# Kernel tuning notes

Measured on AMD Instinct MI355X. Metric: run time of the kernel, lower is better.

## Reference

```python
import jax, jax.numpy as jnp
import numpy as np

B, S, W = 32, 128, 20
WV, CV = 50000, 128
WD, CE = 300, 50
KS = (2, 3, 4, 5)
NF = 64
TOTF = NF * len(KS)
CF = 300
H = 512
L = 9
LP = L + 2
START, END = L, L + 1
NEG = -10000.0


def setup_inputs():
    key = jax.random.key(0)
    ks = jax.random.split(key, 40)
    def nrm(i, shape, scale=0.1):
        return jax.random.normal(ks[i], shape, dtype=jnp.float32) * scale
    inp = {}
    inp['token_ids'] = jax.random.randint(ks[0], (B, S), 0, WV)
    inp['char_ids'] = jax.random.randint(ks[1], (B, S, W), 0, CV)
    lens = jnp.sort(jax.random.randint(ks[2], (B,), S // 2, S + 1))[::-1]
    inp['lens'] = lens.astype(jnp.int32)
    inp['labels'] = jax.random.randint(ks[3], (B, S), 0, L)
    inp['word_embed'] = nrm(4, (WV, WD))
    inp['char_embed'] = nrm(5, (CV, CE))
    for j, k in enumerate(KS):
        inp['conv_w%d' % k] = nrm(6 + j, (k, CE, NF))
        inp['conv_b%d' % k] = nrm(10 + j, (NF,))
    inp['ff_w'] = nrm(14, (CF, TOTF))
    inp['ff_b'] = nrm(15, (CF,))
    inp['wgate_w'] = nrm(16, (WD, WD))
    inp['cgate_w'] = nrm(17, (CF, CF))
    inp['gate_w'] = nrm(18, (WD, WD))
    inp['wih_f'] = nrm(19, (4 * H, WD))
    inp['whh_f'] = nrm(20, (4 * H, H))
    inp['b_f'] = nrm(21, (4 * H,))
    inp['wih_b'] = nrm(22, (4 * H, WD))
    inp['whh_b'] = nrm(23, (4 * H, H))
    inp['b_b'] = nrm(24, (4 * H,))
    inp['out_w'] = nrm(25, (L, 2 * H))
    inp['out_b'] = nrm(26, (L,))
    inp['trn'] = nrm(27, (LP, LP))
    return inp


def _char_cnn(char_ids, char_embed, convs):
    x = char_embed[char_ids.reshape(-1, W)]  # [B*S, W, CE]
    feats = []
    for w, b in convs:
        y = jax.lax.conv_general_dilated(x, w, (1,), 'VALID',
                                         dimension_numbers=('NWC', 'WIO', 'NWC')) + b
        feats.append(jnp.max(jax.nn.relu(y), axis=1))  # max over time -> [B*S, NF]
    return jnp.concatenate(feats, axis=1)  # [B*S, TOTF]


def _run_lstm(x, mask, wih, whh, b, reverse):
    # x [B,S,D], mask bool [B,S]; padded steps freeze state and emit zeros (packed-seq semantics)
    xg = jnp.einsum('bsd,gd->bsg', x, wih) + b  # [B,S,4H]
    xg_t = jnp.swapaxes(xg, 0, 1)               # [S,B,4H]
    m_t = jnp.swapaxes(mask, 0, 1)[..., None]   # [S,B,1]
    h0 = jnp.zeros((x.shape[0], H), x.dtype)
    def step(carry, inp):
        h, c = carry
        g_t, m = inp
        g = g_t + h @ whh.T
        i, f, gg, o = jnp.split(g, 4, axis=-1)  # torch gate order i,f,g,o
        cn = jax.nn.sigmoid(f) * c + jax.nn.sigmoid(i) * jnp.tanh(gg)
        hn = jax.nn.sigmoid(o) * jnp.tanh(cn)
        h = jnp.where(m, hn, h)
        c = jnp.where(m, cn, c)
        return (h, c), jnp.where(m, hn, 0.0)
    _, out = jax.lax.scan(step, (h0, h0), (xg_t, m_t), reverse=reverse)
    return jnp.swapaxes(out, 0, 1)  # [B,S,H]


def _crf_norm(logits, mask, trn):
    # logits [B,S,LP]; trn[i,j] = score(prev=j -> next=i)
    alpha = logits[:, 0] + trn[:, START][None, :]
    lt = jnp.swapaxes(logits, 0, 1)[1:]                 # [S-1,B,LP]
    mt = jnp.swapaxes(mask, 0, 1)[1:][..., None]        # [S-1,B,1]
    def step(alpha, inp):
        lg, m = inp
        new = jax.scipy.special.logsumexp(alpha[:, None, :] + trn[None], axis=2) + lg
        return jnp.where(m, new, alpha), None
    alpha, _ = jax.lax.scan(step, alpha, (lt, mt))
    return jax.scipy.special.logsumexp(alpha + trn[END][None, :], axis=1)


def _crf_gold(logits, labels, lens, mask, trn):
    fm = mask.astype(logits.dtype)
    emit = jnp.take_along_axis(logits, labels[..., None], axis=2)[..., 0]
    emit = jnp.sum(emit * fm, axis=1)
    trans = trn[labels[:, 1:], labels[:, :-1]] * fm[:, 1:]
    first = trn[labels[:, 0], START]
    last_lab = jnp.take_along_axis(labels, (lens - 1)[:, None], axis=1)[:, 0]
    return emit + jnp.sum(trans, axis=1) + first + trn[END, last_lab]


def reference(token_ids, char_ids, lens, labels, word_embed, char_embed,
              conv_w2, conv_b2, conv_w3, conv_b3, conv_w4, conv_b4, conv_w5, conv_b5,
              ff_w, ff_b, wgate_w, cgate_w, gate_w,
              wih_f, whh_f, b_f, wih_b, whh_b, b_b, out_w, out_b, trn):
    word_in = word_embed[token_ids]                               # [B,S,WD]
    convs = [(conv_w2, conv_b2), (conv_w3, conv_b3), (conv_w4, conv_b4), (conv_w5, conv_b5)]
    ch = _char_cnn(char_ids, char_embed, convs)                   # [B*S,TOTF]
    char_in = (ch @ ff_w.T + ff_b).reshape(B, S, CF)              # CharCNNFF output
    g = jax.nn.sigmoid(jnp.tanh(word_in @ wgate_w.T + char_in @ cgate_w.T) @ gate_w.T)
    feats = g * word_in + (1.0 - g) * char_in                     # gated fusion (dropout = eval identity)
    mask = jnp.arange(S)[None, :] < lens[:, None]                 # [B,S] bool
    hf = _run_lstm(feats, mask, wih_f, whh_f, b_f, False)
    hb = _run_lstm(feats, mask, wih_b, whh_b, b_b, True)
    lstm_out = jnp.concatenate([hf, hb], axis=-1)                 # [B,S,2H]
    logits = lstm_out @ out_w.T + out_b                           # [B,S,L]
    pads = jnp.full((B, S, 2), NEG, logits.dtype)
    logits = jnp.concatenate([logits, pads], axis=2)              # pad_logits -> [B,S,LP]
    norm = _crf_norm(logits, mask, trn)
    gold = _crf_gold(logits, labels, lens, mask, trn)
    loglik = gold - norm
    return (loglik, logits)
```

## Files before the change

### kernel.cpp

```cpp
#include <hip/hip_runtime.h>

#define NB    32
#define SEQ   128
#define WCH   20
#define CED   50
#define NFLT  64
#define WDIM  300
#define HD    512
#define NWORD 4096
#define LPAD  11
#define NEGV  -10000.0f
#define LSTM_BLOCKS 16

typedef float f32x4 __attribute__((ext_vector_type(4)));
typedef __bf16 bf16x8 __attribute__((ext_vector_type(8)));
typedef unsigned short u16x8 __attribute__((ext_vector_type(8)));

static __device__ __forceinline__ unsigned short f2bf(float f) {
  unsigned u = __builtin_bit_cast(unsigned, f);
  u += 0x7fffu + ((u >> 16) & 1u);
  return (unsigned short)(u >> 16);
}
static __device__ __forceinline__ float bf2f(unsigned short s) {
  unsigned u = ((unsigned)s) << 16;
  return __builtin_bit_cast(float, u);
}
static __device__ __forceinline__ float sigf(float x) { return 1.0f / (1.0f + expf(-x)); }
static __device__ __forceinline__ void unpk(unsigned u, float& a, float& b) {
  a = bf2f((unsigned short)(u & 0xffffu));
  b = bf2f((unsigned short)(u >> 16));
}

__global__ __launch_bounds__(256) void conv_kernel(
    const int* __restrict__ char_ids, const float* __restrict__ char_embed,
    const float* __restrict__ w2, const float* __restrict__ b2,
    const float* __restrict__ w3, const float* __restrict__ b3,
    const float* __restrict__ w4, const float* __restrict__ b4,
    const float* __restrict__ w5, const float* __restrict__ b5,
    float* __restrict__ ch)
{
  __shared__ __align__(16) float xT[CED][WCH];
  int wi = blockIdx.x;
  int tid = threadIdx.x;
  for (int e = tid; e < WCH * CED; e += 256) {
    int p = e / CED, c = e - p * CED;
    int cid = char_ids[wi * WCH + p];
    xT[c][p] = char_embed[cid * CED + c];
  }
  __syncthreads();
  int w = tid >> 6, f = tid & 63;
  int k = w + 2;
  int P = WCH - k + 1;
  const float* cw = (w == 0) ? w2 : (w == 1) ? w3 : (w == 2) ? w4 : w5;
  const float* cb = (w == 0) ? b2 : (w == 1) ? b3 : (w == 2) ? b4 : b5;
  float acc[19];
  #pragma unroll
  for (int p = 0; p < 19; p++) acc[p] = 0.f;
  for (int c = 0; c < CED; c++) {
    float xr[20];
    const float4* rowp = (const float4*)&xT[c][0];
    #pragma unroll
    for (int q = 0; q < 5; q++) {
      float4 v = rowp[q];
      xr[4*q+0] = v.x; xr[4*q+1] = v.y; xr[4*q+2] = v.z; xr[4*q+3] = v.w;
    }
    #pragma unroll
    for (int dw = 0; dw < 5; dw++) {
      if (dw < k) {
        float wv = cw[(dw * CED + c) * NFLT + f];
        #pragma unroll
        for (int p = 0; p < 19; p++) {
          if (p < P) acc[p] += xr[p + dw] * wv;
        }
      }
    }
  }
  float m = acc[0];
  #pragma unroll
  for (int p = 1; p < 19; p++) if (p < P) m = fmaxf(m, acc[p]);
  ch[wi * 256 + w * 64 + f] = fmaxf(0.f, m + cb[f]);
}

__global__ void gather_word_kernel(const int* __restrict__ token_ids,
                                   const float* __restrict__ word_embed,
                                   float* __restrict__ word_in)
{
  int idx = blockIdx.x * 256 + threadIdx.x;
  if (idx < NWORD * WDIM) {
    int i = idx / WDIM, c = idx - i * WDIM;
    word_in[idx] = word_embed[token_ids[i] * WDIM + c];
  }
}

__global__ __launch_bounds__(256) void gemm_bt_kernel(
    const float* __restrict__ A, const float* __restrict__ Bw,
    const float* __restrict__ bias, const float* __restrict__ Cin,
    float* __restrict__ Cout, unsigned short* __restrict__ Cbf,
    int M, int N, int K, int act, int gridN)
{
  __shared__ __align__(16) unsigned short As[128 * 32];
  __shared__ __align__(16) unsigned short Bs[128 * 32];
  int bid = blockIdx.x;
  int tm = bid / gridN, tn = bid - tm * gridN;
  int m0 = tm * 128, n0 = tn * 128;
  int tid = threadIdx.x;
  int lane = tid & 63, w = tid >> 6;
  int wr = (w >> 1) * 64, wc = (w & 1) * 64;
  f32x4 acc[4][4] = {};
  int fr = lane & 15, fk = (lane >> 4) * 8;

  for (int k0 = 0; k0 < K; k0 += 32) {
    __syncthreads();
    #pragma unroll
    for (int i = 0; i < 16; i++) {
      int e = tid + i * 256;
      int r = e >> 5, c = e & 31;
      int kx = k0 + c;
      int ra = m0 + r, rb = n0 + r;
      float av = (kx < K && ra < M) ? A[(size_t)ra * K + kx] : 0.f;
      float bv = (kx < K && rb < N) ? Bw[(size_t)rb * K + kx] : 0.f;
      As[r * 32 + c] = f2bf(av);
      Bs[r * 32 + c] = f2bf(bv);
    }
    __syncthreads();
    bf16x8 a[4], b[4];
    #pragma unroll
    for (int mt = 0; mt < 4; mt++)
      a[mt] = *(const bf16x8*)&As[(wr + mt * 16 + fr) * 32 + fk];
    #pragma unroll
    for (int nt = 0; nt < 4; nt++)
      b[nt] = *(const bf16x8*)&Bs[(wc + nt * 16 + fr) * 32 + fk];
    #pragma unroll
    for (int mt = 0; mt < 4; mt++)
      #pragma unroll
      for (int nt = 0; nt < 4; nt++)
        acc[mt][nt] = __builtin_amdgcn_mfma_f32_16x16x32_bf16(a[mt], b[nt], acc[mt][nt], 0, 0, 0);
  }

  #pragma unroll
  for (int mt = 0; mt < 4; mt++) {
    #pragma unroll
    for (int nt = 0; nt < 4; nt++) {
      #pragma unroll
      for (int j = 0; j < 4; j++) {
        int row = m0 + wr + mt * 16 + (lane >> 4) * 4 + j;
        int col = n0 + wc + nt * 16 + (lane & 15);
        if (row < M && col < N) {
          float v = acc[mt][nt][j];
          if (Cin)  v += Cin[(size_t)row * N + col];
          if (bias) v += bias[col];
          if (act == 1)      v = tanhf(v);
          else if (act == 2) v = sigf(v);
          if (Cbf) Cbf[(size_t)row * N + col] = f2bf(v);
          else     Cout[(size_t)row * N + col] = v;
        }
      }
    }
  }
}

__global__ void feats_kernel(const float* __restrict__ g, const float* __restrict__ word_in,
                             const float* __restrict__ char_in, float* __restrict__ feats,
                             unsigned* __restrict__ flags)
{
  if (blockIdx.x == 0 && threadIdx.x < 32)
    __hip_atomic_store(&flags[threadIdx.x], 0u, __ATOMIC_RELAXED, __HIP_MEMORY_SCOPE_AGENT);
  int idx = blockIdx.x * 256 + threadIdx.x;
  if (idx < NWORD * WDIM) {
    float gg = g[idx];
    feats[idx] = gg * word_in[idx] + (1.f - gg) * char_in[idx];
  }
}

__global__ __launch_bounds__(1024, 4) void lstm_kernel(
    const unsigned short* __restrict__ xg_f, const unsigned short* __restrict__ xg_b,
    const float* __restrict__ whh_f, const float* __restrict__ whh_b,
    const int* __restrict__ lens,
    float* __restrict__ lstm_out, unsigned short* __restrict__ h_glob,
    unsigned* __restrict__ flags)
{
  int bid = blockIdx.x;
  int dir = bid >> 3, sl = bid & 7;
  int hs0 = sl << 6;
  int tid = threadIdx.x, lane = tid & 63, w = tid >> 6;
  int g = w & 3, hc = w >> 2;
  int l15 = lane & 15, lhi = lane >> 4;
  const unsigned short* xg = dir ? xg_b : xg_f;
  const float* whh = dir ? whh_b : whh_f;
  unsigned short* hg = h_glob + dir * (2 * NB * HD);
  unsigned* myflags = flags + dir * 16;

  bf16x8 wf[16];
  {
    const float* src = whh + (size_t)(g * HD + hs0 + hc * 16 + l15) * HD;
    #pragma unroll
    for (int kk = 0; kk < 16; kk++) {
      int kb = kk * 32 + lhi * 8;
      u16x8 t;
      #pragma unroll
      for (int j2 = 0; j2 < 8; j2++) t[j2] = f2bf(src[kb + j2]);
      wf[kk] = __builtin_bit_cast(bf16x8, t);
    }
  }

  __shared__ __align__(16) unsigned short hS[32 * 512];
  __shared__ float Gs[NB][260];

  int b = tid >> 5, hp = tid & 31;
  int j0 = 2 * hp, j1 = j0 + 1;
  int mylen = lens[b];
  float c0 = 0.f, c1 = 0.f;
  float hprev0 = 0.f, hprev1 = 0.f;

  for (int s = 0; s < SEQ; s++) {
    int t = dir ? (SEQ - 1 - s) : s;

    if (s > 0) {
      if (tid == 0) {
        unsigned long long* fp = (unsigned long long*)myflags;
        for (;;) {
          unsigned long long f0 = __hip_atomic_load(fp + 0, __ATOMIC_RELAXED, __HIP_MEMORY_SCOPE_AGENT);
          unsigned long long f1 = __hip_atomic_load(fp + 1, __ATOMIC_RELAXED, __HIP_MEMORY_SCOPE_AGENT);
          unsigned long long f2 = __hip_atomic_load(fp + 2, __ATOMIC_RELAXED, __HIP_MEMORY_SCOPE_AGENT);
          unsigned long long f3 = __hip_atomic_load(fp + 3, __ATOMIC_RELAXED, __HIP_MEMORY_SCOPE_AGENT);
          unsigned mn = (unsigned)f0;
          mn = min(mn, (unsigned)(f0 >> 32));
          mn = min(mn, (unsigned)f1); mn = min(mn, (unsigned)(f1 >> 32));
          mn = min(mn, (unsigned)f2); mn = min(mn, (unsigned)(f2 >> 32));
          mn = min(mn, (unsigned)f3); mn = min(mn, (unsigned)(f3 >> 32));
          if (mn >= (unsigned)s) break;
          __builtin_amdgcn_s_sleep(1);
        }
      }
      __syncthreads();
      {
        unsigned long long* hq = (unsigned long long*)(hg + (s & 1) * (NB * HD));
        unsigned long long v0 = __hip_atomic_load(hq + tid * 4 + 0, __ATOMIC_RELAXED, __HIP_MEMORY_SCOPE_AGENT);
        unsigned long long v1 = __hip_atomic_load(hq + tid * 4 + 1, __ATOMIC_RELAXED, __HIP_MEMORY_SCOPE_AGENT);
        unsigned long long v2 = __hip_atomic_load(hq + tid * 4 + 2, __ATOMIC_RELAXED, __HIP_MEMORY_SCOPE_AGENT);
        unsigned long long v3 = __hip_atomic_load(hq + tid * 4 + 3, __ATOMIC_RELAXED, __HIP_MEMORY_SCOPE_AGENT);
        int row = tid >> 5;
        int colb = (tid & 31) * 32;
        unsigned sw = (unsigned)((row & 7) << 4);
        char* base = (char*)hS + row * 1024;
        uint4 q0, q1;
        q0.x = (unsigned)v0; q0.y = (unsigned)(v0 >> 32); q0.z = (unsigned)v1; q0.w = (unsigned)(v1 >> 32);
        q1.x = (unsigned)v2; q1.y = (unsigned)(v2 >> 32); q1.z = (unsigned)v3; q1.w = (unsigned)(v3 >> 32);
        *(uint4*)(base + ((unsigned)colb ^ sw)) = q0;
        *(uint4*)(base + ((unsigned)(colb + 16) ^ sw)) = q1;
      }
    }

    unsigned xpi, xpf, xpg, xpo;
    {
      const unsigned* x32 = (const unsigned*)xg;
      size_t base2 = (((size_t)(b * SEQ + t)) * 2048 + hs0 + j0) >> 1;
      xpi = x32[base2 + 0];
      xpf = x32[base2 + 256];
      xpg = x32[base2 + 512];
      xpo = x32[base2 + 768];
    }

    f32x4 acc0 = {0.f, 0.f, 0.f, 0.f};
    f32x4 acc1 = {0.f, 0.f, 0.f, 0.f};
    if (s > 0) {
      __syncthreads();
      #pragma unroll
      for (int kk = 0; kk < 16; kk++) {
        int cb = kk * 64 + lhi * 16;
        int r0 = l15, r1 = 16 + l15;
        unsigned sw = (unsigned)((r0 & 7) << 4);
        bf16x8 a0 = *(const bf16x8*)((const char*)hS + ((unsigned)(r0 * 1024 + cb) ^ sw));
        bf16x8 a1 = *(const bf16x8*)((const char*)hS + ((unsigned)(r1 * 1024 + cb) ^ sw));
        acc0 = __builtin_amdgcn_mfma_f32_16x16x32_bf16(a0, wf[kk], acc0, 0, 0, 0);
        acc1 = __builtin_amdgcn_mfma_f32_16x16x32_bf16(a1, wf[kk], acc1, 0, 0, 0);
      }
    }
    #pragma unroll
    for (int j2 = 0; j2 < 4; j2++) {
      int b0 = lhi * 4 + j2;
      Gs[b0][g * 64 + hc * 16 + l15] = acc0[j2];
      Gs[16 + b0][g * 64 + hc * 16 + l15] = acc1[j2];
    }
    __syncthreads();

    float xi0, xi1, xf0, xf1, xG0, xG1, xo0, xo1;
    unpk(xpi, xi0, xi1); unpk(xpf, xf0, xf1); unpk(xpg, xG0, xG1); unpk(xpo, xo0, xo1);

    float i0 = sigf(xi0 + Gs[b][j0]),        i1 = sigf(xi1 + Gs[b][j1]);
    float f0 = sigf(xf0 + Gs[b][64 + j0]),   f1 = sigf(xf1 + Gs[b][64 + j1]);
    float g0 = tanhf(xG0 + Gs[b][128 + j0]), g1 = tanhf(xG1 + Gs[b][128 + j1]);
    float o0 = sigf(xo0 + Gs[b][192 + j0]),  o1 = sigf(xo1 + Gs[b][192 + j1]);
    float cn0 = f0 * c0 + i0 * g0;
    float cn1 = f1 * c1 + i1 * g1;
    float hn0 = o0 * tanhf(cn0);
    float hn1 = o1 * tanhf(cn1);

    bool mk = (t < mylen);
    if (mk) { c0 = cn0; c1 = cn1; }
    float hk0 = mk ? hn0 : hprev0, hk1 = mk ? hn1 : hprev1;
    hprev0 = hk0; hprev1 = hk1;

    {
      unsigned* hdst32 = (unsigned*)(hg + ((s & 1) ^ 1) * (NB * HD));
      unsigned pk = (unsigned)f2bf(hk0) | ((unsigned)f2bf(hk1) << 16);
      __hip_atomic_store(&hdst32[(b * HD + hs0 + j0) >> 1], pk, __ATOMIC_RELAXED, __HIP_MEMORY_SCOPE_AGENT);
    }
    size_t obase = ((size_t)(b * SEQ + t)) * 1024 + dir * HD + hs0 + j0;
    *(float2*)&lstm_out[obase] = make_float2(mk ? hn0 : 0.f, mk ? hn1 : 0.f);

    __syncthreads();
    if (tid == 0)
      __hip_atomic_store(&myflags[sl], (unsigned)(s + 1), __ATOMIC_RELAXED, __HIP_MEMORY_SCOPE_AGENT);
  }
}

__global__ __launch_bounds__(64) void logits_kernel(
    const float* __restrict__ lstm_out, const float* __restrict__ out_w,
    const float* __restrict__ out_b, float* __restrict__ lg)
{
  int rw = blockIdx.x, j = threadIdx.x;
  const float* row = lstm_out + (size_t)rw * 1024;
  float s[9];
  #pragma unroll
  for (int l = 0; l < 9; l++) s[l] = 0.f;
  for (int e = j; e < 1024; e += 64) {
    float x = row[e];
    #pragma unroll
    for (int l = 0; l < 9; l++) s[l] += x * out_w[l * 1024 + e];
  }
  #pragma unroll
  for (int l = 0; l < 9; l++) {
    #pragma unroll
    for (int off = 32; off > 0; off >>= 1) s[l] += __shfl_xor(s[l], off);
  }
  float v = NEGV;
  if (j < 9) {
    float r = (j==0)?s[0]:(j==1)?s[1]:(j==2)?s[2]:(j==3)?s[3]:(j==4)?s[4]:
              (j==5)?s[5]:(j==6)?s[6]:(j==7)?s[7]:s[8];
    v = r + out_b[j];
  }
  if (j < LPAD) lg[(size_t)rw * LPAD + j] = v;
}

__global__ __launch_bounds__(64) void crf_gold_kernel(
    const float* __restrict__ lg, const int* __restrict__ labels,
    const int* __restrict__ lens, const float* __restrict__ trn, float* __restrict__ gold)
{
  int b = blockIdx.x, j = threadIdx.x;
  int len = lens[b];
  const int* lab = labels + b * SEQ;
  const float* l0 = lg + (size_t)b * SEQ * LPAD;
  float s = 0.f;
  for (int t = j; t < SEQ; t += 64) {
    if (t < len) {
      s += l0[t * LPAD + lab[t]];
      if (t >= 1) s += trn[lab[t] * LPAD + lab[t - 1]];
    }
  }
  #pragma unroll
  for (int off = 32; off > 0; off >>= 1) s += __shfl_xor(s, off);
  if (j == 0) {
    s += trn[lab[0] * LPAD + 9];
    s += trn[10 * LPAD + lab[len - 1]];
    gold[b] = s;
  }
}

__global__ __launch_bounds__(64) void crf_norm_kernel(
    const float* __restrict__ lg, const int* __restrict__ lens,
    const float* __restrict__ trn, const float* __restrict__ gold, float* __restrict__ out_ll)
{
  int b = blockIdx.x, i = threadIdx.x;
  int len = lens[b];
  const float* l0 = lg + (size_t)b * SEQ * LPAD;
  bool act = (i < LPAD);
  float trow[LPAD];
  #pragma unroll
  for (int jj = 0; jj < LPAD; jj++) trow[jj] = act ? trn[i * LPAD + jj] : 0.f;
  float alpha = act ? (l0[i] + trow[9]) : -1e30f;

  for (int t = 1; t < SEQ; t++) {
    float vj[LPAD];
    #pragma unroll
    for (int jj = 0; jj < LPAD; jj++) vj[jj] = __shfl(alpha, jj) + trow[jj];
    float mx = vj[0];
    #pragma unroll
    for (int jj = 1; jj < LPAD; jj++) mx = fmaxf(mx, vj[jj]);
    float sum = 0.f;
    #pragma unroll
    for (int jj = 0; jj < LPAD; jj++) sum += expf(vj[jj] - mx);
    float lgv = act ? l0[t * LPAD + i] : 0.f;
    float nw = mx + logf(sum) + lgv;
    if (act && t < len) alpha = nw;
  }
  float vj[LPAD];
  #pragma unroll
  for (int jj = 0; jj < LPAD; jj++) vj[jj] = __shfl(alpha, jj) + trn[10 * LPAD + jj];
  float mx = vj[0];
  #pragma unroll
  for (int jj = 1; jj < LPAD; jj++) mx = fmaxf(mx, vj[jj]);
  float sum = 0.f;
  #pragma unroll
  for (int jj = 0; jj < LPAD; jj++) sum += expf(vj[jj] - mx);
  if (i == 0) out_ll[b] = gold[b] - (mx + logf(sum));
}

extern "C" void kernel_launch(void* const* d_in, const int* in_sizes, int n_in,
                              void* d_out, int out_size, void* d_ws, size_t ws_size,
                              hipStream_t stream)
{
  (void)in_sizes; (void)n_in; (void)out_size; (void)ws_size;
  const int*   token_ids = (const int*)d_in[0];
  const int*   char_ids  = (const int*)d_in[1];
  const int*   lens      = (const int*)d_in[2];
  const int*   labels    = (const int*)d_in[3];
  const float* word_embed= (const float*)d_in[4];
  const float* char_embed= (const float*)d_in[5];
  const float* w2 = (const float*)d_in[6];  const float* cb2 = (const float*)d_in[7];
  const float* w3 = (const float*)d_in[8];  const float* cb3 = (const float*)d_in[9];
  const float* w4 = (const float*)d_in[10]; const float* cb4 = (const float*)d_in[11];
  const float* w5 = (const float*)d_in[12]; const float* cb5 = (const float*)d_in[13];
  const float* ff_w = (const float*)d_in[14]; const float* ff_b = (const float*)d_in[15];
  const float* wgate_w = (const float*)d_in[16];
  const float* cgate_w = (const float*)d_in[17];
  const float* gate_w  = (const float*)d_in[18];
  const float* wih_f = (const float*)d_in[19]; const float* whh_f = (const float*)d_in[20];
  const float* b_f   = (const float*)d_in[21];
  const float* wih_b = (const float*)d_in[22]; const float* whh_b = (const float*)d_in[23];
  const float* b_b   = (const float*)d_in[24];
  const float* out_w = (const float*)d_in[25]; const float* out_b = (const float*)d_in[26];
  const float* trn   = (const float*)d_in[27];

  char* ws = (char*)d_ws;
  size_t off = 0;
  auto alloc = [&](size_t bytes) { void* p = ws + off; off += (bytes + 255) & ~(size_t)255; return p; };
  float* ch       = (float*)alloc((size_t)NWORD * 256 * 4);
  float* word_in  = (float*)alloc((size_t)NWORD * WDIM * 4);
  float* char_in  = (float*)alloc((size_t)NWORD * WDIM * 4);
  float* t1       = (float*)alloc((size_t)NWORD * WDIM * 4);
  float* gbuf     = (float*)alloc((size_t)NWORD * WDIM * 4);
  float* feats    = (float*)alloc((size_t)NWORD * WDIM * 4);
  unsigned short* xgf = (unsigned short*)alloc((size_t)NWORD * 2048 * 2);
  unsigned short* xgb = (unsigned short*)alloc((size_t)NWORD * 2048 * 2);
  float* lstm_o   = (float*)alloc((size_t)NWORD * 1024 * 4);
  unsigned short* hglob = (unsigned short*)alloc((size_t)2 * 2 * NB * HD * 2);
  float* gold     = (float*)alloc((size_t)NB * 4);
  unsigned* flags = (unsigned*)alloc(256);

  float* outp   = (float*)d_out;
  float* loglik = outp;
  float* logits = outp + NB;

  conv_kernel<<<NWORD, 256, 0, stream>>>(char_ids, char_embed, w2, cb2, w3, cb3, w4, cb4, w5, cb5, ch);
  gather_word_kernel<<<(NWORD * WDIM + 255) / 256, 256, 0, stream>>>(token_ids, word_embed, word_in);
  gemm_bt_kernel<<<32 * 3, 256, 0, stream>>>(ch, ff_w, ff_b, nullptr, char_in, nullptr, NWORD, 300, 256, 0, 3);
  gemm_bt_kernel<<<32 * 3, 256, 0, stream>>>(word_in, wgate_w, nullptr, nullptr, t1, nullptr, NWORD, 300, 300, 0, 3);
  gemm_bt_kernel<<<32 * 3, 256, 0, stream>>>(char_in, cgate_w, nullptr, t1, t1, nullptr, NWORD, 300, 300, 1, 3);
  gemm_bt_kernel<<<32 * 3, 256, 0, stream>>>(t1, gate_w, nullptr, nullptr, gbuf, nullptr, NWORD, 300, 300, 2, 3);
  feats_kernel<<<(NWORD * WDIM + 255) / 256, 256, 0, stream>>>(gbuf, word_in, char_in, feats, flags);
  gemm_bt_kernel<<<32 * 16, 256, 0, stream>>>(feats, wih_f, b_f, nullptr, nullptr, xgf, NWORD, 2048, 300, 0, 16);
  gemm_bt_kernel<<<32 * 16, 256, 0, stream>>>(feats, wih_b, b_b, nullptr, nullptr, xgb, NWORD, 2048, 300, 0, 16);
  {
    void* args[] = { (void*)&xgf, (void*)&xgb, (void*)&whh_f, (void*)&whh_b,
                     (void*)&lens, (void*)&lstm_o, (void*)&hglob, (void*)&flags };
    hipLaunchCooperativeKernel((void*)lstm_kernel, dim3(LSTM_BLOCKS), dim3(1024), args, 0, stream);
  }
  logits_kernel<<<NWORD, 64, 0, stream>>>(lstm_o, out_w, out_b, logits);
  crf_gold_kernel<<<NB, 64, 0, stream>>>(logits, labels, lens, trn, gold);
  crf_norm_kernel<<<NB, 64, 0, stream>>>(logits, lens, trn, gold, loglik);
}
```

Baseline: 1.535 ms.

## Restructure LSTM kernel to 512 threads with 32x32 MFMA and prefetched gate inputs

The recurrent LSTM kernel drops from 1024 to 512 threads per block. Each wave now covers 32 hidden units with 32x32x16 bf16 MFMAs, holding twice as many weight fragments in registers, and each thread computes 4 hidden units with vector Gs reads and 64-bit h stores. The next step's gate pre-activations are prefetched after the flag store, taking that load off the sequential critical path. The GEMM tile loader also switches to float4 loads with packed bf16 stores to cut load instructions, at the cost of higher register pressure in the LSTM kernel.

```diff
diff --git a/kernel.cpp b/kernel.cpp
--- a/kernel.cpp
+++ b/kernel.cpp
@@ -13,8 +13,11 @@
 #define LSTM_BLOCKS 16
 
 typedef float f32x4 __attribute__((ext_vector_type(4)));
+typedef float f32x16 __attribute__((ext_vector_type(16)));
 typedef __bf16 bf16x8 __attribute__((ext_vector_type(8)));
 typedef unsigned short u16x8 __attribute__((ext_vector_type(8)));
+typedef unsigned short u16x4 __attribute__((ext_vector_type(4)));
+typedef unsigned long long ull;
 
 static __device__ __forceinline__ unsigned short f2bf(float f) {
   unsigned u = __builtin_bit_cast(unsigned, f);
@@ -26,10 +29,6 @@
   return __builtin_bit_cast(float, u);
 }
 static __device__ __forceinline__ float sigf(float x) { return 1.0f / (1.0f + expf(-x)); }
-static __device__ __forceinline__ void unpk(unsigned u, float& a, float& b) {
-  a = bf2f((unsigned short)(u & 0xffffu));
-  b = bf2f((unsigned short)(u >> 16));
-}
 
 __global__ __launch_bounds__(256) void conv_kernel(
     const int* __restrict__ char_ids, const float* __restrict__ char_embed,
@@ -112,15 +111,21 @@
   for (int k0 = 0; k0 < K; k0 += 32) {
     __syncthreads();
     #pragma unroll
-    for (int i = 0; i < 16; i++) {
-      int e = tid + i * 256;
-      int r = e >> 5, c = e & 31;
-      int kx = k0 + c;
+    for (int i = 0; i < 4; i++) {
+      int idx = tid + i * 256;
+      int r = idx >> 3, c4 = idx & 7;
+      int kx = k0 + c4 * 4;
       int ra = m0 + r, rb = n0 + r;
-      float av = (kx < K && ra < M) ? A[(size_t)ra * K + kx] : 0.f;
-      float bv = (kx < K && rb < N) ? Bw[(size_t)rb * K + kx] : 0.f;
-      As[r * 32 + c] = f2bf(av);
-      Bs[r * 32 + c] = f2bf(bv);
+      f32x4 av = {0.f,0.f,0.f,0.f}, bv = {0.f,0.f,0.f,0.f};
+      if (kx < K) {
+        if (ra < M) av = *(const f32x4*)&A[(size_t)ra * K + kx];
+        if (rb < N) bv = *(const f32x4*)&Bw[(size_t)rb * K + kx];
+      }
+      u16x4 ap, bp;
+      #pragma unroll
+      for (int j = 0; j < 4; j++) { ap[j] = f2bf(av[j]); bp[j] = f2bf(bv[j]); }
+      *(u16x4*)&As[r * 32 + c4 * 4] = ap;
+      *(u16x4*)&Bs[r * 32 + c4 * 4] = bp;
     }
     __syncthreads();
     bf16x8 a[4], b[4];
@@ -172,7 +177,7 @@
   }
 }
 
-__global__ __launch_bounds__(1024, 4) void lstm_kernel(
+__global__ __launch_bounds__(512, 2) void lstm_kernel(
     const unsigned short* __restrict__ xg_f, const unsigned short* __restrict__ xg_b,
     const float* __restrict__ whh_f, const float* __restrict__ whh_b,
     const int* __restrict__ lens,
@@ -184,45 +189,52 @@
   int hs0 = sl << 6;
   int tid = threadIdx.x, lane = tid & 63, w = tid >> 6;
   int g = w & 3, hc = w >> 2;
-  int l15 = lane & 15, lhi = lane >> 4;
+  int l31 = lane & 31, le = lane >> 5;
   const unsigned short* xg = dir ? xg_b : xg_f;
   const float* whh = dir ? whh_b : whh_f;
   unsigned short* hg = h_glob + dir * (2 * NB * HD);
   unsigned* myflags = flags + dir * 16;
 
-  bf16x8 wf[16];
+  bf16x8 wf[32];
   {
-    const float* src = whh + (size_t)(g * HD + hs0 + hc * 16 + l15) * HD;
-    #pragma unroll
-    for (int kk = 0; kk < 16; kk++) {
-      int kb = kk * 32 + lhi * 8;
-      u16x8 t;
+    const float* src = whh + (size_t)(g * HD + hs0 + hc * 32 + l31) * HD + le * 8;
+    #pragma unroll
+    for (int kk = 0; kk < 32; kk++) {
+      u16x8 tv;
       #pragma unroll
-      for (int j2 = 0; j2 < 8; j2++) t[j2] = f2bf(src[kb + j2]);
-      wf[kk] = __builtin_bit_cast(bf16x8, t);
-    }
-  }
-
-  __shared__ __align__(16) unsigned short hS[32 * 512];
+      for (int j = 0; j < 8; j++) tv[j] = f2bf(src[kk * 16 + j]);
+      wf[kk] = __builtin_bit_cast(bf16x8, tv);
+    }
+  }
+
+  __shared__ __align__(16) unsigned short hS[16384];
   __shared__ float Gs[NB][260];
 
-  int b = tid >> 5, hp = tid & 31;
-  int j0 = 2 * hp, j1 = j0 + 1;
+  int b = tid >> 4;
+  int u = (tid & 15) << 2;
+  int srow = tid >> 4, sq = tid & 15;
   int mylen = lens[b];
-  float c0 = 0.f, c1 = 0.f;
-  float hprev0 = 0.f, hprev1 = 0.f;
+  float c4[4] = {0.f,0.f,0.f,0.f}, hp4[4] = {0.f,0.f,0.f,0.f};
+
+  ull xq0, xq1, xq2, xq3;
+  {
+    int t0 = dir ? (SEQ - 1) : 0;
+    const ull* xp = (const ull*)&xg[((size_t)(b * SEQ + t0)) * 2048 + hs0 + u];
+    xq0 = xp[0]; xq1 = xp[128]; xq2 = xp[256]; xq3 = xp[384];
+  }
 
   for (int s = 0; s < SEQ; s++) {
     int t = dir ? (SEQ - 1 - s) : s;
+    f32x16 acc0 = {}, acc1 = {};
 
     if (s > 0) {
       if (tid == 0) {
-        unsigned long long* fp = (unsigned long long*)myflags;
+        const ull* fp = (const ull*)myflags;
         for (;;) {
-          unsigned long long f0 = __hip_atomic_load(fp + 0, __ATOMIC_RELAXED, __HIP_MEMORY_SCOPE_AGENT);
-          unsigned long long f1 = __hip_atomic_load(fp + 1, __ATOMIC_RELAXED, __HIP_MEMORY_SCOPE_AGENT);
-          unsigned long long f2 = __hip_atomic_load(fp + 2, __ATOMIC_RELAXED, __HIP_MEMORY_SCOPE_AGENT);
-          unsigned long long f3 = __hip_atomic_load(fp + 3, __ATOMIC_RELAXED, __HIP_MEMORY_SCOPE_AGENT);
+          ull f0 = __hip_atomic_load(fp + 0, __ATOMIC_RELAXED, __HIP_MEMORY_SCOPE_AGENT);
+          ull f1 = __hip_atomic_load(fp + 1, __ATOMIC_RELAXED, __HIP_MEMORY_SCOPE_AGENT);
+          ull f2 = __hip_atomic_load(fp + 2, __ATOMIC_RELAXED, __HIP_MEMORY_SCOPE_AGENT);
+          ull f3 = __hip_atomic_load(fp + 3, __ATOMIC_RELAXED, __HIP_MEMORY_SCOPE_AGENT);
           unsigned mn = (unsigned)f0;
           mn = min(mn, (unsigned)(f0 >> 32));
           mn = min(mn, (unsigned)f1); mn = min(mn, (unsigned)(f1 >> 32));
@@ -234,84 +246,82 @@
       }
       __syncthreads();
       {
-        unsigned long long* hq = (unsigned long long*)(hg + (s & 1) * (NB * HD));
-        unsigned long long v0 = __hip_atomic_load(hq + tid * 4 + 0, __ATOMIC_RELAXED, __HIP_MEMORY_SCOPE_AGENT);
-        unsigned long long v1 = __hip_atomic_load(hq + tid * 4 + 1, __ATOMIC_RELAXED, __HIP_MEMORY_SCOPE_AGENT);
-        unsigned long long v2 = __hip_atomic_load(hq + tid * 4 + 2, __ATOMIC_RELAXED, __HIP_MEMORY_SCOPE_AGENT);
-        unsigned long long v3 = __hip_atomic_load(hq + tid * 4 + 3, __ATOMIC_RELAXED, __HIP_MEMORY_SCOPE_AGENT);
-        int row = tid >> 5;
-        int colb = (tid & 31) * 32;
-        unsigned sw = (unsigned)((row & 7) << 4);
-        char* base = (char*)hS + row * 1024;
-        uint4 q0, q1;
-        q0.x = (unsigned)v0; q0.y = (unsigned)(v0 >> 32); q0.z = (unsigned)v1; q0.w = (unsigned)(v1 >> 32);
-        q1.x = (unsigned)v2; q1.y = (unsigned)(v2 >> 32); q1.z = (unsigned)v3; q1.w = (unsigned)(v3 >> 32);
-        *(uint4*)(base + ((unsigned)colb ^ sw)) = q0;
-        *(uint4*)(base + ((unsigned)(colb + 16) ^ sw)) = q1;
-      }
-    }
-
-    unsigned xpi, xpf, xpg, xpo;
-    {
-      const unsigned* x32 = (const unsigned*)xg;
-      size_t base2 = (((size_t)(b * SEQ + t)) * 2048 + hs0 + j0) >> 1;
-      xpi = x32[base2 + 0];
-      xpf = x32[base2 + 256];
-      xpg = x32[base2 + 512];
-      xpo = x32[base2 + 768];
-    }
-
-    f32x4 acc0 = {0.f, 0.f, 0.f, 0.f};
-    f32x4 acc1 = {0.f, 0.f, 0.f, 0.f};
-    if (s > 0) {
+        const ull* hq = (const ull*)(hg + (s & 1) * (NB * HD));
+        ull v[8];
+        #pragma unroll
+        for (int i = 0; i < 8; i++)
+          v[i] = __hip_atomic_load(hq + srow * 128 + sq * 8 + i, __ATOMIC_RELAXED, __HIP_MEMORY_SCOPE_AGENT);
+        int rs = ((srow ^ (sq & 7)) & 31) << 4;
+        #pragma unroll
+        for (int e2 = 0; e2 < 4; e2++) {
+          int kk = 2 * sq + (e2 >> 1), e = e2 & 1;
+          uint4 qv;
+          qv.x = (unsigned)v[2*e2];     qv.y = (unsigned)(v[2*e2] >> 32);
+          qv.z = (unsigned)v[2*e2+1];   qv.w = (unsigned)(v[2*e2+1] >> 32);
+          *(uint4*)((char*)hS + (((kk * 2 + e) << 9) + rs)) = qv;
+        }
+      }
       __syncthreads();
       #pragma unroll
-      for (int kk = 0; kk < 16; kk++) {
-        int cb = kk * 64 + lhi * 16;
-        int r0 = l15, r1 = 16 + l15;
-        unsigned sw = (unsigned)((r0 & 7) << 4);
-        bf16x8 a0 = *(const bf16x8*)((const char*)hS + ((unsigned)(r0 * 1024 + cb) ^ sw));
-        bf16x8 a1 = *(const bf16x8*)((const char*)hS + ((unsigned)(r1 * 1024 + cb) ^ sw));
-        acc0 = __builtin_amdgcn_mfma_f32_16x16x32_bf16(a0, wf[kk], acc0, 0, 0, 0);
-        acc1 = __builtin_amdgcn_mfma_f32_16x16x32_bf16(a1, wf[kk], acc1, 0, 0, 0);
-      }
-    }
-    #pragma unroll
-    for (int j2 = 0; j2 < 4; j2++) {
-      int b0 = lhi * 4 + j2;
-      Gs[b0][g * 64 + hc * 16 + l15] = acc0[j2];
-      Gs[16 + b0][g * 64 + hc * 16 + l15] = acc1[j2];
+      for (int kk = 0; kk < 32; kk += 2) {
+        int rs = ((l31 ^ ((kk >> 1) & 7)) & 31) << 4;
+        int a0off = ((kk * 2 + le) << 9) + rs;
+        int a1off = ((kk * 2 + 2 + le) << 9) + rs;
+        bf16x8 a0 = *(const bf16x8*)((const char*)hS + a0off);
+        bf16x8 a1 = *(const bf16x8*)((const char*)hS + a1off);
+        acc0 = __builtin_amdgcn_mfma_f32_32x32x16_bf16(a0, wf[kk], acc0, 0, 0, 0);
+        acc1 = __builtin_amdgcn_mfma_f32_32x32x16_bf16(a1, wf[kk+1], acc1, 0, 0, 0);
+      }
+    }
+
+    #pragma unroll
+    for (int r = 0; r < 16; r++) {
+      int bb = (r & 3) + 8 * (r >> 2) + 4 * le;
+      Gs[bb][g * 64 + hc * 32 + l31] = acc0[r] + acc1[r];
     }
     __syncthreads();
 
-    float xi0, xi1, xf0, xf1, xG0, xG1, xo0, xo1;
-    unpk(xpi, xi0, xi1); unpk(xpf, xf0, xf1); unpk(xpg, xG0, xG1); unpk(xpo, xo0, xo1);
-
-    float i0 = sigf(xi0 + Gs[b][j0]),        i1 = sigf(xi1 + Gs[b][j1]);
-    float f0 = sigf(xf0 + Gs[b][64 + j0]),   f1 = sigf(xf1 + Gs[b][64 + j1]);
-    float g0 = tanhf(xG0 + Gs[b][128 + j0]), g1 = tanhf(xG1 + Gs[b][128 + j1]);
-    float o0 = sigf(xo0 + Gs[b][192 + j0]),  o1 = sigf(xo1 + Gs[b][192 + j1]);
-    float cn0 = f0 * c0 + i0 * g0;
-    float cn1 = f1 * c1 + i1 * g1;
-    float hn0 = o0 * tanhf(cn0);
-    float hn1 = o1 * tanhf(cn1);
-
+    f32x4 gi  = *(const f32x4*)&Gs[b][u];
+    f32x4 gfv = *(const f32x4*)&Gs[b][64 + u];
+    f32x4 ggv = *(const f32x4*)&Gs[b][128 + u];
+    f32x4 gov = *(const f32x4*)&Gs[b][192 + u];
     bool mk = (t < mylen);
-    if (mk) { c0 = cn0; c1 = cn1; }
-    float hk0 = mk ? hn0 : hprev0, hk1 = mk ? hn1 : hprev1;
-    hprev0 = hk0; hprev1 = hk1;
-
+    f32x4 outv;
+    ull hpk = 0;
+    #pragma unroll
+    for (int j = 0; j < 4; j++) {
+      float xi = bf2f((unsigned short)(xq0 >> (16*j)));
+      float xf = bf2f((unsigned short)(xq1 >> (16*j)));
+      float xG = bf2f((unsigned short)(xq2 >> (16*j)));
+      float xo = bf2f((unsigned short)(xq3 >> (16*j)));
+      float iv = sigf(xi + gi[j]);
+      float fv = sigf(xf + gfv[j]);
+      float Gv = tanhf(xG + ggv[j]);
+      float ov = sigf(xo + gov[j]);
+      float cn = fv * c4[j] + iv * Gv;
+      float hn = ov * tanhf(cn);
+      if (mk) c4[j] = cn;
+      float hk = mk ? hn : hp4[j];
+      hp4[j] = hk;
+      outv[j] = mk ? hn : 0.f;
+      hpk |= ((ull)f2bf(hk)) << (16*j);
+    }
+    size_t obase = ((size_t)(b * SEQ + t)) * 1024 + dir * HD + hs0 + u;
+    *(f32x4*)&lstm_out[obase] = outv;
     {
-      unsigned* hdst32 = (unsigned*)(hg + ((s & 1) ^ 1) * (NB * HD));
-      unsigned pk = (unsigned)f2bf(hk0) | ((unsigned)f2bf(hk1) << 16);
-      __hip_atomic_store(&hdst32[(b * HD + hs0 + j0) >> 1], pk, __ATOMIC_RELAXED, __HIP_MEMORY_SCOPE_AGENT);
-    }
-    size_t obase = ((size_t)(b * SEQ + t)) * 1024 + dir * HD + hs0 + j0;
-    *(float2*)&lstm_out[obase] = make_float2(mk ? hn0 : 0.f, mk ? hn1 : 0.f);
+      ull* hd = (ull*)(hg + ((s & 1) ^ 1) * (NB * HD));
+      __hip_atomic_store(&hd[(b * HD + hs0 + u) >> 2], hpk, __ATOMIC_RELAXED, __HIP_MEMORY_SCOPE_AGENT);
+    }
 
     __syncthreads();
     if (tid == 0)
       __hip_atomic_store(&myflags[sl], (unsigned)(s + 1), __ATOMIC_RELAXED, __HIP_MEMORY_SCOPE_AGENT);
+
+    if (s + 1 < SEQ) {
+      int tn = dir ? (SEQ - 2 - s) : (s + 1);
+      const ull* xp = (const ull*)&xg[((size_t)(b * SEQ + tn)) * 2048 + hs0 + u];
+      xq0 = xp[0]; xq1 = xp[128]; xq2 = xp[256]; xq3 = xp[384];
+    }
   }
 }
 
@@ -464,7 +474,7 @@
   {
     void* args[] = { (void*)&xgf, (void*)&xgb, (void*)&whh_f, (void*)&whh_b,
                      (void*)&lens, (void*)&lstm_o, (void*)&hglob, (void*)&flags };
-    hipLaunchCooperativeKernel((void*)lstm_kernel, dim3(LSTM_BLOCKS), dim3(1024), args, 0, stream);
+    hipLaunchCooperativeKernel((void*)lstm_kernel, dim3(LSTM_BLOCKS), dim3(512), args, 0, stream);
   }
   logits_kernel<<<NWORD, 64, 0, stream>>>(lstm_o, out_w, out_b, logits);
   crf_gold_kernel<<<NB, 64, 0, stream>>>(logits, labels, lens, trn, gold);
```

Measured after the change: 1.303 ms. 1.18x faster.
